# Optimization experiments

Hardware: AMD Instinct MI355X
Metric: run time of the kernel (lower is better)

## Reference

```python
import jax, jax.numpy as jnp
import numpy as np

K = 3          # kernel size
STRIDE = 1
PAD = 1
GROUPS = 32    # GroupNorm groups
EPS = 1e-5


def setup_inputs() -> dict:
    key = jax.random.key(0)
    ks = jax.random.split(key, 6)
    B, Cin, H, W, Cout = 4, 256, 64, 64, 256
    K2 = K * K
    x = jax.random.normal(ks[0], (B, Cin, H, W), jnp.float32)
    offset = jax.random.normal(ks[1], (B, 2 * K2, H, W), jnp.float32)
    mask = jax.random.uniform(ks[2], (B, K2, H, W), jnp.float32)
    weight = jax.random.normal(ks[3], (Cout, Cin, K, K), jnp.float32) * (1.0 / np.sqrt(Cin * K2))
    bias = jnp.zeros((Cout,), jnp.float32)
    gamma = jnp.ones((Cout,), jnp.float32)   # constant_init(norm, 1)
    beta = jnp.zeros((Cout,), jnp.float32)   # bias=0
    return {"x": x, "offset": offset, "mask": mask, "weight": weight,
            "bias": bias, "gamma": gamma, "beta": beta}


def _modulated_deform_conv(x, offset, mask, weight, bias):
    """DCNv2: bilinear-sample x at learned offsets, modulate by mask, conv-accumulate."""
    B, Cin, H, W = x.shape
    Cout = weight.shape[0]
    K2 = K * K
    Ho = (H + 2 * PAD - K) // STRIDE + 1
    Wo = (W + 2 * PAD - K) // STRIDE + 1

    # base sampling grid per kernel point: [K2, Ho, Wo]
    ky, kx = jnp.meshgrid(jnp.arange(K), jnp.arange(K), indexing='ij')
    ky = ky.reshape(K2).astype(jnp.float32)
    kx = kx.reshape(K2).astype(jnp.float32)
    hs = (jnp.arange(Ho) * STRIDE - PAD).astype(jnp.float32)
    ws = (jnp.arange(Wo) * STRIDE - PAD).astype(jnp.float32)

    off = offset.reshape(B, K2, 2, Ho, Wo)  # interleaved (dy, dx) per kernel point
    y = ky[None, :, None, None] + hs[None, None, :, None] + off[:, :, 0]   # [B,K2,Ho,Wo]
    xc = kx[None, :, None, None] + ws[None, None, None, :] + off[:, :, 1]  # [B,K2,Ho,Wo]

    y0 = jnp.floor(y)
    x0 = jnp.floor(xc)
    dy = y - y0
    dx = xc - x0
    y0i = y0.astype(jnp.int32)
    x0i = x0.astype(jnp.int32)

    x_flat = x.reshape(B, Cin, H * W)

    def corner(yi, xi, w):
        # corner-wise zero padding outside the image (matches mmcv bilinear)
        valid = (yi >= 0) & (yi <= H - 1) & (xi >= 0) & (xi <= W - 1)
        idx = jnp.clip(yi, 0, H - 1) * W + jnp.clip(xi, 0, W - 1)  # [B,K2,Ho,Wo]
        idx_f = idx.reshape(B, -1)
        v = jax.vmap(lambda xf, i: xf[:, i])(x_flat, idx_f)  # [B, Cin, K2*Ho*Wo]
        wv = (w * valid.astype(w.dtype)).reshape(B, 1, -1)
        return v * wv

    val = (corner(y0i,     x0i,     (1 - dy) * (1 - dx))
         + corner(y0i,     x0i + 1, (1 - dy) * dx)
         + corner(y0i + 1, x0i,     dy * (1 - dx))
         + corner(y0i + 1, x0i + 1, dy * dx))
    val = val.reshape(B, Cin, K2, Ho, Wo) * mask[:, None]  # modulate

    w_r = weight.reshape(Cout, Cin, K2)
    out = jnp.einsum('bckhw,ock->bohw', val, w_r) + bias[None, :, None, None]
    return out


def _group_norm(x, gamma, beta):
    B, C, H, W = x.shape
    g = x.reshape(B, GROUPS, C // GROUPS, H, W)
    mu = g.mean(axis=(2, 3, 4), keepdims=True)
    var = ((g - mu) ** 2).mean(axis=(2, 3, 4), keepdims=True)
    g = (g - mu) * jax.lax.rsqrt(var + EPS)
    return g.reshape(B, C, H, W) * gamma[None, :, None, None] + beta[None, :, None, None]


def reference(x, offset, mask, weight, bias, gamma, beta):
    out = _modulated_deform_conv(x, offset, mask, weight, bias)
    out = _group_norm(out, gamma, beta)
    return jax.nn.relu(out)
```

## Files before the change

kernel.cpp:

```cpp
#include <hip/hip_runtime.h>
#include <math.h>

#define BB    4
#define CIN   256
#define HH    64
#define WWID  64
#define COUT  256
#define KKS   3
#define K2    9
#define PADV  1
#define HWSZ  4096
#define GROUPS 32
#define CPG   8
#define EPSV  1e-5f
#define NKC   36

typedef __attribute__((ext_vector_type(8))) short bf16x8;
typedef __attribute__((ext_vector_type(4))) float f32x4;
typedef __attribute__((ext_vector_type(2))) float f32x2;

__device__ __forceinline__ unsigned short f2bf(float f) {
    unsigned u = __float_as_uint(f);
    u = (u + 0x7fffu + ((u >> 16) & 1u)) >> 16;
    return (unsigned short)u;
}
__device__ __forceinline__ f32x2 up2(unsigned q) {
    f32x2 v;
    v.x = __uint_as_float(q << 16);
    v.y = __uint_as_float(q & 0xffff0000u);
    return v;
}
__device__ __forceinline__ unsigned cvtpk(f32x2 f) {
    unsigned r;
    asm("v_cvt_pk_bf16_f32 %0, %1, %2" : "=v"(r) : "v"(f.x), "v"(f.y));
    return r;
}

__global__ __launch_bounds__(256)
void k_pre(const float* __restrict__ x, unsigned short* __restrict__ xh,
           const float* __restrict__ w, unsigned short* __restrict__ wtb,
           float* __restrict__ gstat) {
    int t = threadIdx.x;
    if (blockIdx.x < 64) {
        __shared__ float tile[32][65];
        int hw0 = blockIdx.x * 64;
        int c0  = blockIdx.y * 32;
        int b   = blockIdx.z;
        const float* xp = x + (size_t)b * CIN * HWSZ;
        int col = t & 63, r0 = t >> 6;
        #pragma unroll
        for (int i = 0; i < 8; i++)
            tile[i * 4 + r0][col] = xp[(c0 + i * 4 + r0) * HWSZ + hw0 + col];
        __syncthreads();
        int hw = t >> 2, cq = t & 3;
        union { unsigned short s[8]; uint4 qq; } pk;
        #pragma unroll
        for (int k = 0; k < 8; k++) pk.s[k] = f2bf(tile[cq * 8 + k][hw]);
        *(uint4*)((char*)xh + (((size_t)b * HWSZ + hw0 + hw) * CIN + c0 + cq * 8) * 2) = pk.qq;
    } else {
        if (blockIdx.y == 0 && blockIdx.z == 0)
            for (int i = t; i < BB * GROUPS * 2 + 8; i += 256) gstat[i] = 0.f;
        int idx = (blockIdx.y * 4 + blockIdx.z) * 256 + t;
        int co = idx >> 5, c8 = idx & 31;
        int q  = c8 >> 3;
        int ks = (c8 & 7) >> 2;
        int hf = c8 & 3;
        int lane16 = hf * 16 + (co & 15);
        for (int k2 = 0; k2 < K2; k2++) {
            int kc = k2 * 4 + q;
            union { unsigned short s[8]; uint4 qq; } pk;
            #pragma unroll
            for (int j = 0; j < 8; j++)
                pk.s[j] = f2bf(w[(co * CIN + c8 * 8 + j) * K2 + k2]);
            size_t phys = (size_t)(((co >> 4) * 36 + kc)) * 2048 + ks * 1024 + lane16 * 16;
            *(uint4*)((char*)wtb + phys) = pk.qq;
        }
    }
}

#define GATHER2(garr, gwarr, kn) do { \
    int k2n_ = (kn) >> 2, qn_ = (kn) & 3; \
    int cb_ = (px0 * K2 + k2n_) * 4; \
    int4   ci_ = *(const int4*)&cidx[cb_]; \
    float4 cw_ = *(const float4*)&cwgt[cb_]; \
    gwarr[0] = cw_.x; gwarr[1] = cw_.y; gwarr[2] = cw_.z; gwarr[3] = cw_.w; \
    const char* xq_ = xb + qn_ * 128; \
    garr[0] = *(const uint4*)(xq_ + ci_.x); \
    garr[1] = *(const uint4*)(xq_ + ci_.y); \
    garr[2] = *(const uint4*)(xq_ + ci_.z); \
    garr[3] = *(const uint4*)(xq_ + ci_.w); \
} while (0)

#define ISSUE_A(Ar) do { \
    Ar[0] = *(const bf16x8*)(ap0);        Ar[1] = *(const bf16x8*)(ap0 + 1024); \
    Ar[2] = *(const bf16x8*)(ap1);        Ar[3] = *(const bf16x8*)(ap1 + 1024); \
    Ar[4] = *(const bf16x8*)(ap2);        Ar[5] = *(const bf16x8*)(ap2 + 1024); \
    Ar[6] = *(const bf16x8*)(ap3);        Ar[7] = *(const bf16x8*)(ap3 + 1024); \
    ap0 += 2048; ap1 += 2048; ap2 += 2048; ap3 += 2048; \
} while (0)

#define PACK(garr, gwarr, Bdst) do { \
    f32x2 f0 = {0.f, 0.f}, f1 = {0.f, 0.f}, f2 = {0.f, 0.f}, f3 = {0.f, 0.f}; \
    _Pragma("unroll") \
    for (int c_ = 0; c_ < 4; c_++) { \
        f32x2 wv_ = { gwarr[c_], gwarr[c_] }; \
        f0 = __builtin_elementwise_fma(wv_, up2(garr[c_].x), f0); \
        f1 = __builtin_elementwise_fma(wv_, up2(garr[c_].y), f1); \
        f2 = __builtin_elementwise_fma(wv_, up2(garr[c_].z), f2); \
        f3 = __builtin_elementwise_fma(wv_, up2(garr[c_].w), f3); \
    } \
    uint4 pk_; \
    pk_.x = cvtpk(f0); pk_.y = cvtpk(f1); pk_.z = cvtpk(f2); pk_.w = cvtpk(f3); \
    *(uint4*)&(Bdst)[bofs0] = pk_; \
} while (0)

#define MFMA_STEP(Ar, Bc) do { \
    __builtin_amdgcn_s_setprio(1); \
    _Pragma("unroll") \
    for (int ks_ = 0; ks_ < 2; ks_++) { \
        int up_ = ((ks_ * 4 + hf) ^ skey) * 8; \
        bf16x8 bv_[2]; \
        _Pragma("unroll") \
        for (int ni_ = 0; ni_ < 2; ni_++) \
            bv_[ni_] = *(const bf16x8*)&(Bc)[(wn * 32 + ni_ * 16 + r16) * 64 + up_]; \
        _Pragma("unroll") \
        for (int mi_ = 0; mi_ < 4; mi_++) \
            _Pragma("unroll") \
            for (int ni_ = 0; ni_ < 2; ni_++) \
                acc[mi_][ni_] = __builtin_amdgcn_mfma_f32_16x16x32_bf16( \
                    Ar[mi_ * 2 + ks_], bv_[ni_], acc[mi_][ni_], 0, 0, 0); \
    } \
    __builtin_amdgcn_s_setprio(0); \
} while (0)

#define LGKM_BAR() do { \
    asm volatile("s_waitcnt lgkmcnt(0)\n\ts_barrier" ::: "memory"); \
    __builtin_amdgcn_sched_barrier(0); \
} while (0)

#define BODY(kc, Acur, Anxt, Bcur, Bnxt, gU, gwU, gF, gwF) do { \
    ISSUE_A(Anxt); \
    GATHER2(gF, gwF, (kc) + 2); \
    __builtin_amdgcn_sched_barrier(0); \
    MFMA_STEP(Acur, Bcur); \
    __builtin_amdgcn_sched_barrier(0); \
    PACK(gU, gwU, Bnxt); \
    LGKM_BAR(); \
} while (0)

__global__ __launch_bounds__(512, 2)
void k_conv(const unsigned short* __restrict__ wtb, const unsigned short* __restrict__ xh,
            const float* __restrict__ offset, const float* __restrict__ mask,
            const float* __restrict__ bias, float* __restrict__ out,
            float* __restrict__ gstat) {
    __shared__ __align__(16) unsigned short Bs[2][64 * 64];
    __shared__ __align__(16) int   cidx[64 * K2 * 4];
    __shared__ __align__(16) float cwgt[64 * K2 * 4];
    __shared__ float gs[32], gss[32];

    int lid = blockIdx.x;
    int strip = (lid & 7) * 32 + (lid >> 3);
    int b = strip >> 6;
    int hwbase = (strip & 63) * 64;

    int t = threadIdx.x, w = t >> 6, l = t & 63;
    int r16 = l & 15, hf = l >> 4;
    int skey = r16 & 7;
    int wm = w & 3, wn = w >> 2;

    if (t < 32) { gs[t] = 0.f; gss[t] = 0.f; }

    for (int i = t; i < 64 * K2; i += 512) {
        int px = i / K2, k2 = i - px * K2;
        int hw = hwbase + px;
        int ho = hw >> 6, wo = hw & 63;
        int ky = k2 / KKS, kx = k2 - ky * KKS;
        float dy = offset[((b * (2 * K2) + k2 * 2 + 0) * HWSZ) + hw];
        float dx = offset[((b * (2 * K2) + k2 * 2 + 1) * HWSZ) + hw];
        float m  = mask[(b * K2 + k2) * HWSZ + hw];
        float y  = (float)(ky + ho - PADV) + dy;
        float xc = (float)(kx + wo - PADV) + dx;
        float y0f = floorf(y), x0f = floorf(xc);
        float fy = y - y0f, fx = xc - x0f;
        int y0 = (int)y0f, x0 = (int)x0f;
        int   yy[2] = { y0, y0 + 1 };
        int   xx[2] = { x0, x0 + 1 };
        float wy[2] = { 1.f - fy, fy };
        float wx[2] = { 1.f - fx, fx };
        #pragma unroll
        for (int ii = 0; ii < 2; ii++)
            #pragma unroll
            for (int jj = 0; jj < 2; jj++) {
                int yi = yy[ii], xi = xx[jj];
                bool valid = (yi >= 0) && (yi < HH) && (xi >= 0) && (xi < WWID);
                int yc  = min(max(yi, 0), HH - 1);
                int xcc = min(max(xi, 0), WWID - 1);
                cidx[i * 4 + ii * 2 + jj] = (yc * WWID + xcc) << 9;
                cwgt[i * 4 + ii * 2 + jj] = valid ? (wy[ii] * wx[jj] * m) : 0.f;
            }
    }

    const char* wb = (const char*)wtb + (size_t)l * 16;
    const char* ap0 = wb + (size_t)((wm * 4 + 0) * 36) * 2048;
    const char* ap1 = wb + (size_t)((wm * 4 + 1) * 36) * 2048;
    const char* ap2 = wb + (size_t)((wm * 4 + 2) * 36) * 2048;
    const char* ap3 = wb + (size_t)((wm * 4 + 3) * 36) * 2048;

    int sc  = t & 7;
    int px0 = t >> 3;
    const char* xb = (const char*)xh + (size_t)b * HWSZ * CIN * 2 + sc * 16;
    int bofs0 = px0 * 64 + (sc ^ (px0 & 7)) * 8;

    f32x4 acc[4][2];
    #pragma unroll
    for (int mi = 0; mi < 4; mi++)
        #pragma unroll
        for (int ni = 0; ni < 2; ni++) acc[mi][ni] = (f32x4)0.f;

    __syncthreads();

    uint4 gA[4], gB[4]; float gwA[4], gwB[4];
    bf16x8 Aa[8], Ab[8];
    GATHER2(gA, gwA, 0);
    ISSUE_A(Aa);
    GATHER2(gB, gwB, 1);
    PACK(gA, gwA, Bs[0]);
    LGKM_BAR();

    unsigned short* Bs0 = &Bs[0][0];
    unsigned short* Bs1 = &Bs[1][0];

    for (int kc2 = 0; kc2 < 34; kc2 += 2) {
        BODY(kc2,     Aa, Ab, Bs0, Bs1, gB, gwB, gA, gwA);
        BODY(kc2 + 1, Ab, Aa, Bs1, Bs0, gA, gwA, gB, gwB);
    }
    ISSUE_A(Ab);
    __builtin_amdgcn_sched_barrier(0);
    MFMA_STEP(Aa, Bs0);
    __builtin_amdgcn_sched_barrier(0);
    PACK(gB, gwB, Bs1);
    LGKM_BAR();
    MFMA_STEP(Ab, Bs1);

    float s4[4] = {0,0,0,0}, ss4[4] = {0,0,0,0};
    #pragma unroll
    for (int mi = 0; mi < 4; mi++) {
        #pragma unroll
        for (int r = 0; r < 4; r++) {
            int co = wm * 64 + mi * 16 + hf * 4 + r;
            float bs = bias[co];
            float* orow = out + ((size_t)(b * COUT + co)) * HWSZ;
            #pragma unroll
            for (int ni = 0; ni < 2; ni++) {
                int n = hwbase + wn * 32 + ni * 16 + r16;
                float v = acc[mi][ni][r] + bs;
                orow[n] = v;
                s4[mi] += v; ss4[mi] += v * v;
            }
        }
    }
    int gb = hf >> 1;
    #pragma unroll
    for (int mi = 0; mi < 4; mi++) {
        atomicAdd(&gs [wm * 8 + mi * 2 + gb], s4[mi]);
        atomicAdd(&gss[wm * 8 + mi * 2 + gb], ss4[mi]);
    }
    __syncthreads();
    if (t < 32) {
        atomicAdd(&gstat[(b * GROUPS + t) * 2 + 0], gs[t]);
        atomicAdd(&gstat[(b * GROUPS + t) * 2 + 1], gss[t]);
    }
}

__global__ __launch_bounds__(256)
void k_gnfinal(float* __restrict__ out, const float* __restrict__ gstat,
               const float* __restrict__ gamma, const float* __restrict__ beta) {
    int i4 = blockIdx.x * 256 + threadIdx.x;
    int e  = i4 * 4;
    int c  = (e >> 12) & 255;
    int b  = e >> 20;
    int g  = c >> 3;
    float s  = gstat[((b * GROUPS) + g) * 2 + 0];
    float ss = gstat[((b * GROUPS) + g) * 2 + 1];
    const float inv = 1.f / (float)(CPG * HWSZ);
    float mu  = s * inv;
    float var = ss * inv - mu * mu;
    float rstd = rsqrtf(var + EPSV);
    float ga = gamma[c] * rstd;
    float be = beta[c] - mu * ga;
    float4 v = ((float4*)out)[i4];
    v.x = fmaxf(v.x * ga + be, 0.f);
    v.y = fmaxf(v.y * ga + be, 0.f);
    v.z = fmaxf(v.z * ga + be, 0.f);
    v.w = fmaxf(v.w * ga + be, 0.f);
    ((float4*)out)[i4] = v;
}

extern "C" void kernel_launch(void* const* d_in, const int* in_sizes, int n_in,
                              void* d_out, int out_size, void* d_ws, size_t ws_size,
                              hipStream_t stream) {
    const float* x      = (const float*)d_in[0];
    const float* offset = (const float*)d_in[1];
    const float* mask   = (const float*)d_in[2];
    const float* weight = (const float*)d_in[3];
    const float* bias   = (const float*)d_in[4];
    const float* gamma  = (const float*)d_in[5];
    const float* beta   = (const float*)d_in[6];
    float* out = (float*)d_out;

    unsigned short* xh    = (unsigned short*)d_ws;
    unsigned short* wtb   = xh + (size_t)4194304;
    float*          gstat = (float*)(wtb + (size_t)589824);

    k_pre<<<dim3(65, 8, 4), 256, 0, stream>>>(x, xh, weight, wtb, gstat);
    k_conv<<<256, 512, 0, stream>>>(wtb, xh, offset, mask, bias, out, gstat);
    k_gnfinal<<<(size_t)BB * COUT * HWSZ / 1024, 256, 0, stream>>>(out, gstat, gamma, beta);
}
```

Baseline: 146.2 us.

## Halve pixel tile per block to 32, double grid, split gather across warps

Each block now covers 32 output pixels instead of 64, and the grid doubles to 512 blocks. Each of the 8 warps owns 32 output channels across all 32 pixels. Only the first four warps do the bilinear gather and pack into shared memory. Launch bounds now request 4 blocks per CU to raise occupancy and spread work over more CUs. The trade-off is that each block reloads the full weight matrix, doubling weight traffic, and the gather work sits unevenly on half the warps.

```diff
diff --git a/kernel.cpp b/kernel.cpp
--- a/kernel.cpp
+++ b/kernel.cpp
@@ -94,9 +94,7 @@
 #define ISSUE_A(Ar) do { \
     Ar[0] = *(const bf16x8*)(ap0);        Ar[1] = *(const bf16x8*)(ap0 + 1024); \
     Ar[2] = *(const bf16x8*)(ap1);        Ar[3] = *(const bf16x8*)(ap1 + 1024); \
-    Ar[4] = *(const bf16x8*)(ap2);        Ar[5] = *(const bf16x8*)(ap2 + 1024); \
-    Ar[6] = *(const bf16x8*)(ap3);        Ar[7] = *(const bf16x8*)(ap3 + 1024); \
-    ap0 += 2048; ap1 += 2048; ap2 += 2048; ap3 += 2048; \
+    ap0 += 2048; ap1 += 2048; \
 } while (0)
 
 #define PACK(garr, gwarr, Bdst) do { \
@@ -122,9 +120,9 @@
         bf16x8 bv_[2]; \
         _Pragma("unroll") \
         for (int ni_ = 0; ni_ < 2; ni_++) \
-            bv_[ni_] = *(const bf16x8*)&(Bc)[(wn * 32 + ni_ * 16 + r16) * 64 + up_]; \
+            bv_[ni_] = *(const bf16x8*)&(Bc)[(ni_ * 16 + r16) * 64 + up_]; \
         _Pragma("unroll") \
-        for (int mi_ = 0; mi_ < 4; mi_++) \
+        for (int mi_ = 0; mi_ < 2; mi_++) \
             _Pragma("unroll") \
             for (int ni_ = 0; ni_ < 2; ni_++) \
                 acc[mi_][ni_] = __builtin_amdgcn_mfma_f32_16x16x32_bf16( \
@@ -140,37 +138,37 @@
 
 #define BODY(kc, Acur, Anxt, Bcur, Bnxt, gU, gwU, gF, gwF) do { \
     ISSUE_A(Anxt); \
-    GATHER2(gF, gwF, (kc) + 2); \
+    if (heavy) GATHER2(gF, gwF, (kc) + 2); \
     __builtin_amdgcn_sched_barrier(0); \
     MFMA_STEP(Acur, Bcur); \
     __builtin_amdgcn_sched_barrier(0); \
-    PACK(gU, gwU, Bnxt); \
+    if (heavy) PACK(gU, gwU, Bnxt); \
     LGKM_BAR(); \
 } while (0)
 
-__global__ __launch_bounds__(512, 2)
+__global__ __launch_bounds__(512, 4)
 void k_conv(const unsigned short* __restrict__ wtb, const unsigned short* __restrict__ xh,
             const float* __restrict__ offset, const float* __restrict__ mask,
             const float* __restrict__ bias, float* __restrict__ out,
             float* __restrict__ gstat) {
-    __shared__ __align__(16) unsigned short Bs[2][64 * 64];
-    __shared__ __align__(16) int   cidx[64 * K2 * 4];
-    __shared__ __align__(16) float cwgt[64 * K2 * 4];
+    __shared__ __align__(16) unsigned short Bs[2][32 * 64];
+    __shared__ __align__(16) int   cidx[32 * K2 * 4];
+    __shared__ __align__(16) float cwgt[32 * K2 * 4];
     __shared__ float gs[32], gss[32];
 
     int lid = blockIdx.x;
-    int strip = (lid & 7) * 32 + (lid >> 3);
-    int b = strip >> 6;
-    int hwbase = (strip & 63) * 64;
+    int strip = (lid & 7) * 64 + (lid >> 3);
+    int b = strip >> 7;
+    int hwbase = (strip & 127) * 32;
 
     int t = threadIdx.x, w = t >> 6, l = t & 63;
     int r16 = l & 15, hf = l >> 4;
     int skey = r16 & 7;
-    int wm = w & 3, wn = w >> 2;
+    bool heavy = (w < 4);
 
     if (t < 32) { gs[t] = 0.f; gss[t] = 0.f; }
 
-    for (int i = t; i < 64 * K2; i += 512) {
+    for (int i = t; i < 32 * K2; i += 512) {
         int px = i / K2, k2 = i - px * K2;
         int hw = hwbase + px;
         int ho = hw >> 6, wo = hw & 63;
@@ -201,30 +199,30 @@
     }
 
     const char* wb = (const char*)wtb + (size_t)l * 16;
-    const char* ap0 = wb + (size_t)((wm * 4 + 0) * 36) * 2048;
-    const char* ap1 = wb + (size_t)((wm * 4 + 1) * 36) * 2048;
-    const char* ap2 = wb + (size_t)((wm * 4 + 2) * 36) * 2048;
-    const char* ap3 = wb + (size_t)((wm * 4 + 3) * 36) * 2048;
+    const char* ap0 = wb + (size_t)((w * 2 + 0) * 36) * 2048;
+    const char* ap1 = wb + (size_t)((w * 2 + 1) * 36) * 2048;
 
     int sc  = t & 7;
     int px0 = t >> 3;
     const char* xb = (const char*)xh + (size_t)b * HWSZ * CIN * 2 + sc * 16;
     int bofs0 = px0 * 64 + (sc ^ (px0 & 7)) * 8;
 
-    f32x4 acc[4][2];
+    f32x4 acc[2][2];
     #pragma unroll
-    for (int mi = 0; mi < 4; mi++)
+    for (int mi = 0; mi < 2; mi++)
         #pragma unroll
         for (int ni = 0; ni < 2; ni++) acc[mi][ni] = (f32x4)0.f;
 
     __syncthreads();
 
     uint4 gA[4], gB[4]; float gwA[4], gwB[4];
-    bf16x8 Aa[8], Ab[8];
-    GATHER2(gA, gwA, 0);
+    bf16x8 Aa[4], Ab[4];
+    if (heavy) GATHER2(gA, gwA, 0);
     ISSUE_A(Aa);
-    GATHER2(gB, gwB, 1);
-    PACK(gA, gwA, Bs[0]);
+    if (heavy) {
+        GATHER2(gB, gwB, 1);
+        PACK(gA, gwA, Bs[0]);
+    }
     LGKM_BAR();
 
     unsigned short* Bs0 = &Bs[0][0];
@@ -238,21 +236,21 @@
     __builtin_amdgcn_sched_barrier(0);
     MFMA_STEP(Aa, Bs0);
     __builtin_amdgcn_sched_barrier(0);
-    PACK(gB, gwB, Bs1);
+    if (heavy) PACK(gB, gwB, Bs1);
     LGKM_BAR();
     MFMA_STEP(Ab, Bs1);
 
-    float s4[4] = {0,0,0,0}, ss4[4] = {0,0,0,0};
+    float s4[2] = {0,0}, ss4[2] = {0,0};
     #pragma unroll
-    for (int mi = 0; mi < 4; mi++) {
+    for (int mi = 0; mi < 2; mi++) {
         #pragma unroll
         for (int r = 0; r < 4; r++) {
-            int co = wm * 64 + mi * 16 + hf * 4 + r;
+            int co = w * 32 + mi * 16 + hf * 4 + r;
             float bs = bias[co];
             float* orow = out + ((size_t)(b * COUT + co)) * HWSZ;
             #pragma unroll
             for (int ni = 0; ni < 2; ni++) {
-                int n = hwbase + wn * 32 + ni * 16 + r16;
+                int n = hwbase + ni * 16 + r16;
                 float v = acc[mi][ni][r] + bs;
                 orow[n] = v;
                 s4[mi] += v; ss4[mi] += v * v;
@@ -261,9 +259,9 @@
     }
     int gb = hf >> 1;
     #pragma unroll
-    for (int mi = 0; mi < 4; mi++) {
-        atomicAdd(&gs [wm * 8 + mi * 2 + gb], s4[mi]);
-        atomicAdd(&gss[wm * 8 + mi * 2 + gb], ss4[mi]);
+    for (int mi = 0; mi < 2; mi++) {
+        atomicAdd(&gs [w * 4 + mi * 2 + gb], s4[mi]);
+        atomicAdd(&gss[w * 4 + mi * 2 + gb], ss4[mi]);
     }
     __syncthreads();
     if (t < 32) {
@@ -313,6 +311,6 @@
     float*          gstat = (float*)(wtb + (size_t)589824);
 
     k_pre<<<dim3(65, 8, 4), 256, 0, stream>>>(x, xh, weight, wtb, gstat);
-    k_conv<<<256, 512, 0, stream>>>(wtb, xh, offset, mask, bias, out, gstat);
+    k_conv<<<512, 512, 0, stream>>>(wtb, xh, offset, mask, bias, out, gstat);
     k_gnfinal<<<(size_t)BB * COUT * HWSZ / 1024, 256, 0, stream>>>(out, gstat, gamma, beta);
 }
```

New measurement: 144.4 us. Within noise of the previous version (-1.3%).
